# Kernel optimization log

Measured on AMD Instinct MI355X. Metric: run time of the kernel, lower is better.

The kernel has to match this reference:

```python
import jax, jax.numpy as jnp
import numpy as np

N0, N1, N2, N3 = 65536, 16384, 4096, 1024
S = 9  # 3x3 kernel -> 9 selections (self + 8 directions)


def _edges(key, n):
    # each node has S incoming edges, one per selection
    src = jax.random.randint(key, (n * S,), 0, n)
    dst = jnp.repeat(jnp.arange(n), S)
    sel = jnp.tile(jnp.arange(S), n)
    return src, dst, sel


def setup_inputs() -> dict:
    key = jax.random.key(0)
    ks = jax.random.split(key, 40)
    inp = {}
    inp["x"] = jax.random.normal(ks[0], (N0, 3), jnp.float32)
    sizes = [N0, N1, N2, N3]
    for l, n in enumerate(sizes):
        src, dst, sel = _edges(ks[1 + l], n)
        inp[f"src{l}"] = src
        inp[f"dst{l}"] = dst
        inp[f"sel{l}"] = sel
        inp[f"interp{l}"] = jax.random.uniform(ks[5 + l], (n * S,), jnp.float32)
    inp["clus0"] = jnp.arange(N0) // 4
    inp["clus1"] = jnp.arange(N1) // 4
    inp["clus2"] = jnp.arange(N2) // 4
    dims = [(3, 3), (3, 64), (64, 64), (64, 128), (128, 128), (128, 256), (256, 256), (256, 256), (256, 256), (256, 512)]
    for i, (ci, co) in enumerate(dims):
        kw = ks[10 + 2 * i]
        kb = ks[11 + 2 * i]
        if i == 0:  # conv1 is kernel_size=1 -> single weight matrix
            inp["W1"] = jax.random.normal(kw, (ci, co), jnp.float32) / np.sqrt(ci).astype(np.float32)
        else:
            inp[f"W{i + 1}"] = jax.random.normal(kw, (S, ci, co), jnp.float32) / np.sqrt(S * ci).astype(np.float32)
        inp[f"b{i + 1}"] = jax.random.normal(kb, (co,), jnp.float32) * 0.01
    return inp


def _sel_conv(x, src, dst, sel, interp, W, b):
    # message = interp * x[src]; routed to (dst, selection) bucket; per-selection weight
    n = x.shape[0]
    msg = x[src] * interp[:, None]                                  # [E, Cin]
    agg = jax.ops.segment_sum(msg, dst * S + sel, num_segments=n * S)
    agg = agg.reshape(n, S, -1)                                     # [N, S, Cin]
    return jnp.einsum('nsi,sio->no', agg, W) + b


def reference(x, src0, dst0, sel0, interp0, src1, dst1, sel1, interp1,
              src2, dst2, sel2, interp2, src3, dst3, sel3, interp3,
              clus0, clus1, clus2,
              W1, b1, W2, b2, W3, b3, W4, b4, W5, b5,
              W6, b6, W7, b7, W8, b8, W9, b9, W10, b10):
    relu = jax.nn.relu
    out = x @ W1 + b1                                              # conv1 (1x1), no relu
    r11 = relu(_sel_conv(out, src0, dst0, sel0, interp0, W2, b2))
    r12 = relu(_sel_conv(r11, src0, dst0, sel0, interp0, W3, b3))
    p1 = jax.ops.segment_max(r12, clus0, num_segments=N1)
    r21 = relu(_sel_conv(p1, src1, dst1, sel1, interp1, W4, b4))
    r22 = relu(_sel_conv(r21, src1, dst1, sel1, interp1, W5, b5))
    p2 = jax.ops.segment_max(r22, clus1, num_segments=N2)
    r31 = relu(_sel_conv(p2, src2, dst2, sel2, interp2, W6, b6))
    r32 = relu(_sel_conv(r31, src2, dst2, sel2, interp2, W7, b7))
    r33 = relu(_sel_conv(r32, src2, dst2, sel2, interp2, W8, b8))
    r34 = relu(_sel_conv(r33, src2, dst2, sel2, interp2, W9, b9))
    p3 = jax.ops.segment_max(r34, clus2, num_segments=N3)
    r41 = relu(_sel_conv(p3, src3, dst3, sel3, interp3, W10, b10))
    return (r11, r12, p1, r21, r22, p2, r31, r32, r33, r34, p3, r41)
```

## Files before the change

### kernel.cpp

```cpp
#include <hip/hip_runtime.h>
#include <hip/hip_bf16.h>
#include <cstddef>


#define S9 9

typedef __attribute__((ext_vector_type(8))) _Float16 f16x8;
typedef __attribute__((ext_vector_type(4))) float f32x4;

__device__ __forceinline__ unsigned short f2h(float f) {
    _Float16 h = (_Float16)f;
    unsigned short u;
    __builtin_memcpy(&u, &h, 2);
    return u;
}

__device__ void wt_tile(const float* __restrict__ in, unsigned short* __restrict__ out,
                        int K, int N, int t, float (*sm)[33]) {
    const int ktiles = K >> 6, ntiles = N >> 5;
    const int per = ktiles * ntiles;
    const int s = t / per;
    const int rem = t - s * per;
    const int kt = rem % ktiles, nt = rem / ktiles;
    const int k0 = kt * 64, n0 = nt * 32;
    const float* ip = in + (size_t)s * K * N;
    unsigned short* op = out + (size_t)s * N * K;
    const int tx = threadIdx.x & 31;
    const int ty = threadIdx.x >> 5;
#pragma unroll
    for (int r = ty; r < 64; r += 8)
        sm[r][tx] = ip[(size_t)(k0 + r) * N + n0 + tx];
    __syncthreads();
#pragma unroll
    for (int r = ty; r < 32; r += 8) {
        unsigned v = (unsigned)f2h(sm[2 * tx][r]) |
                     ((unsigned)f2h(sm[2 * tx + 1][r]) << 16);
        *(unsigned*)&op[(size_t)(n0 + r) * K + k0 + 2 * tx] = v;
    }
}

__global__ __launch_bounds__(256) void wt_all(
    const float* __restrict__ W2, const float* __restrict__ W3,
    const float* __restrict__ W4, const float* __restrict__ W5,
    const float* __restrict__ W6, const float* __restrict__ W7,
    const float* __restrict__ W8, const float* __restrict__ W9,
    const float* __restrict__ W10,
    unsigned short* o2, unsigned short* o3, unsigned short* o4,
    unsigned short* o5, unsigned short* o6, unsigned short* o7,
    unsigned short* o8, unsigned short* o9, unsigned short* o10) {
    __shared__ float sm[64][33];
    int b = blockIdx.x;
    if (b == 0) {
        for (int idx = threadIdx.x; idx < 64 * 32; idx += 256) {
            const int n = idx >> 5, k = idx & 31;
            o2[n * 32 + k] = (k < 27) ? f2h(W2[k * 64 + n]) : (unsigned short)0;
        }
        return;
    }
    b -= 1;
    if (b < 18)  { wt_tile(W3,  o3,  64,  64,  b, sm); return; }  b -= 18;
    if (b < 36)  { wt_tile(W4,  o4,  64,  128, b, sm); return; }  b -= 36;
    if (b < 72)  { wt_tile(W5,  o5,  128, 128, b, sm); return; }  b -= 72;
    if (b < 144) { wt_tile(W6,  o6,  128, 256, b, sm); return; }  b -= 144;
    if (b < 288) { wt_tile(W7,  o7,  256, 256, b, sm); return; }  b -= 288;
    if (b < 288) { wt_tile(W8,  o8,  256, 256, b, sm); return; }  b -= 288;
    if (b < 288) { wt_tile(W9,  o9,  256, 256, b, sm); return; }  b -= 288;
    wt_tile(W10, o10, 256, 512, b, sm);
}

__global__ void pool4_dual(const float* __restrict__ in, float* __restrict__ outf,
                           _Float16* __restrict__ outh, int total4, int C4) {
    int idx = blockIdx.x * blockDim.x + threadIdx.x;
    if (idx >= total4) return;
    int j = idx / C4;
    int c4 = idx - j * C4;
    const float4* base = (const float4*)in;
    float4 a = base[(size_t)(4 * j + 0) * C4 + c4];
    float4 b = base[(size_t)(4 * j + 1) * C4 + c4];
    float4 c = base[(size_t)(4 * j + 2) * C4 + c4];
    float4 d = base[(size_t)(4 * j + 3) * C4 + c4];
    float4 m;
    m.x = fmaxf(fmaxf(a.x, b.x), fmaxf(c.x, d.x));
    m.y = fmaxf(fmaxf(a.y, b.y), fmaxf(c.y, d.y));
    m.z = fmaxf(fmaxf(a.z, b.z), fmaxf(c.z, d.z));
    m.w = fmaxf(fmaxf(a.w, b.w), fmaxf(c.w, d.w));
    ((float4*)outf)[(size_t)j * C4 + c4] = m;
    uint2 h;
    h.x = (unsigned)f2h(m.x) | ((unsigned)f2h(m.y) << 16);
    h.y = (unsigned)f2h(m.z) | ((unsigned)f2h(m.w) << 16);
    *(uint2*)&outh[((size_t)j * C4 + c4) * 4] = h;
}

template <int BM, int WR, int WC, int MR, int NR>
__global__ __launch_bounds__(256) void selconv_k27(
    const float* __restrict__ x, const int* __restrict__ src,
    const float* __restrict__ interp, const float* __restrict__ W1,
    const float* __restrict__ b1, const _Float16* __restrict__ Wt2,
    const float* __restrict__ bias, float* __restrict__ out,
    _Float16* __restrict__ outh) {
    constexpr int COUT = 64;
    constexpr int LDA = 40;
    __shared__ _Float16 As[BM * LDA];

    const int tid = threadIdx.x;
    const int wave = tid >> 6;
    const int lane = tid & 63;
    const int wr = wave / WC;
    const int wc = wave % WC;
    const int node0 = blockIdx.x * BM;
    const int lm = lane & 15;
    const int kq = lane >> 4;

    const float w00 = W1[0], w01 = W1[1], w02 = W1[2];
    const float w10 = W1[3], w11 = W1[4], w12 = W1[5];
    const float w20 = W1[6], w21 = W1[7], w22 = W1[8];
    const float c0 = b1[0], c1 = b1[1], c2 = b1[2];

    for (int c = tid; c < BM * 5; c += 256) {
        const int ln = c / 5;
        As[ln * LDA + 27 + (c - ln * 5)] = (_Float16)0.f;
    }
    for (int c = tid; c < BM * S9; c += 256) {
        const int ln = c / S9;
        const int s = c - ln * S9;
        const int e = (node0 + ln) * S9 + s;
        const float t = interp[e];
        const float* xr = &x[(size_t)src[e] * 3];
        const float x0 = xr[0], x1 = xr[1], x2 = xr[2];
        const float y0 = fmaf(x0, w00, fmaf(x1, w10, fmaf(x2, w20, c0)));
        const float y1 = fmaf(x0, w01, fmaf(x1, w11, fmaf(x2, w21, c1)));
        const float y2 = fmaf(x0, w02, fmaf(x1, w12, fmaf(x2, w22, c2)));
        As[ln * LDA + s * 3 + 0] = (_Float16)(t * y0);
        As[ln * LDA + s * 3 + 1] = (_Float16)(t * y1);
        As[ln * LDA + s * 3 + 2] = (_Float16)(t * y2);
    }
    __syncthreads();

    f32x4 acc[MR][NR];
    f16x8 bfr[NR];
#pragma unroll
    for (int f = 0; f < NR; ++f) {
        const int col = wc * NR * 16 + f * 16 + lm;
        bfr[f] = *(const f16x8*)(Wt2 + col * 32 + kq * 8);
        const float bv = bias[col];
#pragma unroll
        for (int i = 0; i < MR; ++i) {
            acc[i][f][0] = bv; acc[i][f][1] = bv; acc[i][f][2] = bv; acc[i][f][3] = bv;
        }
    }
#pragma unroll
    for (int i = 0; i < MR; ++i) {
        const f16x8 af =
            *(const f16x8*)&As[(wr * MR * 16 + i * 16 + lm) * LDA + kq * 8];
#pragma unroll
        for (int f = 0; f < NR; ++f)
            acc[i][f] = __builtin_amdgcn_mfma_f32_16x16x32_f16(af, bfr[f],
                                                               acc[i][f], 0, 0, 0);
    }

#pragma unroll
    for (int i = 0; i < MR; ++i)
#pragma unroll
        for (int f = 0; f < NR; ++f) {
            const int col = wc * NR * 16 + f * 16 + lm;
#pragma unroll
            for (int r = 0; r < 4; ++r) {
                const int row = node0 + wr * MR * 16 + i * 16 + kq * 4 + r;
                const float v = fmaxf(acc[i][f][r], 0.f);
                out[(size_t)row * COUT + col] = v;
                outh[(size_t)row * COUT + col] = (_Float16)v;
            }
        }
}

template <int CIN, int COUT, int BM, int BNC, int WR, int WC, int MR, int NR>
__global__ __launch_bounds__(256) void selconv_f16(
    const _Float16* __restrict__ xin, const int* __restrict__ src,
    const float* __restrict__ interp, const _Float16* __restrict__ Wt,
    const float* __restrict__ bias, float* __restrict__ out,
    _Float16* __restrict__ outh) {
    static_assert(WR * WC == 4, "4 waves");
    static_assert(WR * MR * 16 == BM, "BM mismatch");
    static_assert(WC * NR * 16 == BNC, "BNC mismatch");
    constexpr int KSTEPS = CIN / 32;
    constexpr int LDA = CIN + 8;
    constexpr int C8 = CIN / 8;
    constexpr int ITER = (BM * C8) / 256;
    static_assert((BM * C8) % 256 == 0, "staging divisibility");

    __shared__ _Float16 As[BM * LDA];

    const int tid = threadIdx.x;
    const int wave = tid >> 6;
    const int lane = tid & 63;
    const int wr = wave / WC;
    const int wc = wave % WC;
    const int node0 = blockIdx.x * BM;
    const int cb = blockIdx.y * BNC;
    const int lm = lane & 15;
    const int kq = lane >> 4;

    f32x4 acc[MR][NR];
#pragma unroll
    for (int f = 0; f < NR; ++f) {
        const float bv = bias[cb + wc * NR * 16 + f * 16 + lm];
#pragma unroll
        for (int i = 0; i < MR; ++i) {
            acc[i][f][0] = bv; acc[i][f][1] = bv; acc[i][f][2] = bv; acc[i][f][3] = bv;
        }
    }

    const _Float16* __restrict__ Wb =
        Wt + ((size_t)cb + wc * NR * 16 + lm) * CIN + kq * 8;

#pragma unroll 1
    for (int s = 0; s < S9; ++s) {
        int sidx[ITER];
        float ta[ITER];
#pragma unroll
        for (int i = 0; i < ITER; ++i) {
            const int c = tid + i * 256;
            const int ln = c / C8;
            const int e = (node0 + ln) * S9 + s;
            sidx[i] = src[e];
            ta[i] = interp[e];
        }
        f16x8 va[ITER];
#pragma unroll
        for (int i = 0; i < ITER; ++i) {
            const int c = tid + i * 256;
            const int c8 = c - (c / C8) * C8;
            va[i] = *(const f16x8*)&xin[(size_t)sidx[i] * CIN + c8 * 8];
        }
        f16x8 bfr[KSTEPS][NR];
        {
            const _Float16* __restrict__ Wbs = Wb + (size_t)s * COUT * CIN;
#pragma unroll
            for (int kk = 0; kk < KSTEPS; ++kk)
#pragma unroll
                for (int f = 0; f < NR; ++f)
                    bfr[kk][f] = *(const f16x8*)(Wbs + (size_t)f * 16 * CIN + kk * 32);
        }
        __syncthreads();
#pragma unroll
        for (int i = 0; i < ITER; ++i) {
            const int c = tid + i * 256;
            const int ln = c / C8;
            const int c8 = c - ln * C8;
            const _Float16 ht = (_Float16)ta[i];
            f16x8 r;
#pragma unroll
            for (int j = 0; j < 8; ++j) r[j] = va[i][j] * ht;
            *(f16x8*)&As[ln * LDA + c8 * 8] = r;
        }
        __syncthreads();
#pragma unroll
        for (int kk = 0; kk < KSTEPS; ++kk) {
            f16x8 af[MR];
#pragma unroll
            for (int i = 0; i < MR; ++i)
                af[i] = *(const f16x8*)&As[(wr * MR * 16 + i * 16 + lm) * LDA +
                                           kk * 32 + kq * 8];
#pragma unroll
            for (int i = 0; i < MR; ++i)
#pragma unroll
                for (int f = 0; f < NR; ++f)
                    acc[i][f] = __builtin_amdgcn_mfma_f32_16x16x32_f16(
                        af[i], bfr[kk][f], acc[i][f], 0, 0, 0);
        }
    }

#pragma unroll
    for (int i = 0; i < MR; ++i)
#pragma unroll
        for (int f = 0; f < NR; ++f) {
            const int col = cb + wc * NR * 16 + f * 16 + lm;
#pragma unroll
            for (int r = 0; r < 4; ++r) {
                const int row = node0 + wr * MR * 16 + i * 16 + kq * 4 + r;
                const float v = fmaxf(acc[i][f][r], 0.f);
                out[(size_t)row * COUT + col] = v;
                if (outh) outh[(size_t)row * COUT + col] = (_Float16)v;
            }
        }
}

extern "C" void kernel_launch(void* const* d_in, const int* in_sizes, int n_in,
                              void* d_out, int out_size, void* d_ws, size_t ws_size,
                              hipStream_t stream) {
    const float* x = (const float*)d_in[0];
    const int* src0 = (const int*)d_in[1];
    const float* interp0 = (const float*)d_in[4];
    const int* src1 = (const int*)d_in[5];
    const float* interp1 = (const float*)d_in[8];
    const int* src2 = (const int*)d_in[9];
    const float* interp2 = (const float*)d_in[12];
    const int* src3 = (const int*)d_in[13];
    const float* interp3 = (const float*)d_in[16];
    const float* W1 = (const float*)d_in[20];
    const float* b1 = (const float*)d_in[21];
    const float* W2 = (const float*)d_in[22];
    const float* b2 = (const float*)d_in[23];
    const float* W3 = (const float*)d_in[24];
    const float* b3 = (const float*)d_in[25];
    const float* W4 = (const float*)d_in[26];
    const float* b4 = (const float*)d_in[27];
    const float* W5 = (const float*)d_in[28];
    const float* b5 = (const float*)d_in[29];
    const float* W6 = (const float*)d_in[30];
    const float* b6 = (const float*)d_in[31];
    const float* W7 = (const float*)d_in[32];
    const float* b7 = (const float*)d_in[33];
    const float* W8 = (const float*)d_in[34];
    const float* b8 = (const float*)d_in[35];
    const float* W9 = (const float*)d_in[36];
    const float* b9 = (const float*)d_in[37];
    const float* W10 = (const float*)d_in[38];
    const float* b10 = (const float*)d_in[39];

    float* out = (float*)d_out;
    float* r11 = out;
    float* r12 = r11 + (size_t)65536 * 64;
    float* p1 = r12 + (size_t)65536 * 64;
    float* r21 = p1 + (size_t)16384 * 64;
    float* r22 = r21 + (size_t)16384 * 128;
    float* p2 = r22 + (size_t)16384 * 128;
    float* r31 = p2 + (size_t)4096 * 128;
    float* r32 = r31 + (size_t)4096 * 256;
    float* r33 = r32 + (size_t)4096 * 256;
    float* r34 = r33 + (size_t)4096 * 256;
    float* p3 = r34 + (size_t)4096 * 256;
    float* r41 = p3 + (size_t)1024 * 256;

    unsigned short* w16 = (unsigned short*)d_ws;
    unsigned short* Wt2 = w16;
    unsigned short* Wt3 = Wt2 + (size_t)64 * 32;
    unsigned short* Wt4 = Wt3 + (size_t)9 * 64 * 64;
    unsigned short* Wt5 = Wt4 + (size_t)9 * 128 * 64;
    unsigned short* Wt6 = Wt5 + (size_t)9 * 128 * 128;
    unsigned short* Wt7 = Wt6 + (size_t)9 * 256 * 128;
    unsigned short* Wt8 = Wt7 + (size_t)9 * 256 * 256;
    unsigned short* Wt9 = Wt8 + (size_t)9 * 256 * 256;
    unsigned short* Wt10 = Wt9 + (size_t)9 * 256 * 256;
    unsigned short* endw = Wt10 + (size_t)9 * 512 * 256;
    _Float16* a11 = (_Float16*)endw;
    _Float16* ap1 = a11 + (size_t)65536 * 64;
    _Float16* a21 = ap1 + (size_t)16384 * 64;
    _Float16* ap2 = a21 + (size_t)16384 * 128;
    _Float16* a31 = ap2 + (size_t)4096 * 128;
    _Float16* a32 = a31 + (size_t)4096 * 256;
    _Float16* a33 = a32 + (size_t)4096 * 256;
    _Float16* ap3 = a33 + (size_t)4096 * 256;

    wt_all<<<1711, 256, 0, stream>>>(W2, W3, W4, W5, W6, W7, W8, W9, W10,
                                     Wt2, Wt3, Wt4, Wt5, Wt6, Wt7, Wt8, Wt9, Wt10);

    selconv_k27<64, 2, 2, 2, 2><<<dim3(65536 / 64), 256, 0, stream>>>(
        x, src0, interp0, W1, b1, (const _Float16*)Wt2, b2, r11, a11);

    selconv_f16<64, 64, 64, 64, 2, 2, 2, 2><<<dim3(65536 / 64, 1), 256, 0, stream>>>(
        a11, src0, interp0, (const _Float16*)Wt3, b3, r12, nullptr);
    pool4_dual<<<(16384 * 16 + 255) / 256, 256, 0, stream>>>(r12, p1, ap1,
                                                             16384 * 16, 16);

    selconv_f16<64, 128, 32, 64, 2, 2, 1, 2><<<dim3(16384 / 32, 2), 256, 0, stream>>>(
        ap1, src1, interp1, (const _Float16*)Wt4, b4, r21, a21);
    selconv_f16<128, 128, 32, 64, 2, 2, 1, 2><<<dim3(16384 / 32, 2), 256, 0, stream>>>(
        a21, src1, interp1, (const _Float16*)Wt5, b5, r22, nullptr);
    pool4_dual<<<(4096 * 32 + 255) / 256, 256, 0, stream>>>(r22, p2, ap2,
                                                            4096 * 32, 32);

    selconv_f16<128, 256, 32, 64, 2, 2, 1, 2><<<dim3(4096 / 32, 4), 256, 0, stream>>>(
        ap2, src2, interp2, (const _Float16*)Wt6, b6, r31, a31);
    selconv_f16<256, 256, 32, 64, 2, 2, 1, 2><<<dim3(4096 / 32, 4), 256, 0, stream>>>(
        a31, src2, interp2, (const _Float16*)Wt7, b7, r32, a32);
    selconv_f16<256, 256, 32, 64, 2, 2, 1, 2><<<dim3(4096 / 32, 4), 256, 0, stream>>>(
        a32, src2, interp2, (const _Float16*)Wt8, b8, r33, a33);
    selconv_f16<256, 256, 32, 64, 2, 2, 1, 2><<<dim3(4096 / 32, 4), 256, 0, stream>>>(
        a33, src2, interp2, (const _Float16*)Wt9, b9, r34, nullptr);
    pool4_dual<<<(1024 * 64 + 255) / 256, 256, 0, stream>>>(r34, p3, ap3,
                                                            1024 * 64, 64);

    selconv_f16<256, 512, 16, 64, 1, 4, 1, 1><<<dim3(1024 / 16, 8), 256, 0, stream>>>(
        ap3, src3, interp3, (const _Float16*)Wt10, b10, r41, nullptr);
}
```

Before: 430.5 us.

## Gather MFMA operands directly into registers and fuse max-pool into conv epilogue

Removes the shared-memory staging and both barriers in the selection conv kernel. Each lane now gathers its A-fragment rows straight from global memory, scales them by interp in registers, and prefetches the next selection's src and interp values. The separate pool4 kernels are dropped: the 4 accumulator rows a lane holds (kq*4..+3) are max-reduced in the epilogue to write the pooled fp32 and fp16 outputs. Tile sizes are also unified to BM=64, which cuts grid sizes on the small layers (16 or 64 row blocks) and may reduce occupancy. The uncoalesced per-lane gathers (16-byte chunks per lane) could cost memory efficiency.

Result: no change. 433.0 us (+0.6%).

```diff
diff --git a/kernel.cpp b/kernel.cpp
--- a/kernel.cpp
+++ b/kernel.cpp
@@ -68,29 +68,6 @@
     wt_tile(W10, o10, 256, 512, b, sm);
 }
 
-__global__ void pool4_dual(const float* __restrict__ in, float* __restrict__ outf,
-                           _Float16* __restrict__ outh, int total4, int C4) {
-    int idx = blockIdx.x * blockDim.x + threadIdx.x;
-    if (idx >= total4) return;
-    int j = idx / C4;
-    int c4 = idx - j * C4;
-    const float4* base = (const float4*)in;
-    float4 a = base[(size_t)(4 * j + 0) * C4 + c4];
-    float4 b = base[(size_t)(4 * j + 1) * C4 + c4];
-    float4 c = base[(size_t)(4 * j + 2) * C4 + c4];
-    float4 d = base[(size_t)(4 * j + 3) * C4 + c4];
-    float4 m;
-    m.x = fmaxf(fmaxf(a.x, b.x), fmaxf(c.x, d.x));
-    m.y = fmaxf(fmaxf(a.y, b.y), fmaxf(c.y, d.y));
-    m.z = fmaxf(fmaxf(a.z, b.z), fmaxf(c.z, d.z));
-    m.w = fmaxf(fmaxf(a.w, b.w), fmaxf(c.w, d.w));
-    ((float4*)outf)[(size_t)j * C4 + c4] = m;
-    uint2 h;
-    h.x = (unsigned)f2h(m.x) | ((unsigned)f2h(m.y) << 16);
-    h.y = (unsigned)f2h(m.z) | ((unsigned)f2h(m.w) << 16);
-    *(uint2*)&outh[((size_t)j * C4 + c4) * 4] = h;
-}
-
 template <int BM, int WR, int WC, int MR, int NR>
 __global__ __launch_bounds__(256) void selconv_k27(
     const float* __restrict__ x, const int* __restrict__ src,
@@ -173,22 +150,19 @@
         }
 }
 
-template <int CIN, int COUT, int BM, int BNC, int WR, int WC, int MR, int NR>
-__global__ __launch_bounds__(256) void selconv_f16(
+template <int CIN, int COUT, int BM, int BNC, int WR, int WC, int MR, int NR,
+          bool POOL>
+__global__ __launch_bounds__(256) void selconv_dir(
     const _Float16* __restrict__ xin, const int* __restrict__ src,
     const float* __restrict__ interp, const _Float16* __restrict__ Wt,
     const float* __restrict__ bias, float* __restrict__ out,
-    _Float16* __restrict__ outh) {
+    _Float16* __restrict__ outh, float* __restrict__ pout,
+    _Float16* __restrict__ ph) {
     static_assert(WR * WC == 4, "4 waves");
     static_assert(WR * MR * 16 == BM, "BM mismatch");
     static_assert(WC * NR * 16 == BNC, "BNC mismatch");
     constexpr int KSTEPS = CIN / 32;
-    constexpr int LDA = CIN + 8;
-    constexpr int C8 = CIN / 8;
-    constexpr int ITER = (BM * C8) / 256;
-    static_assert((BM * C8) % 256 == 0, "staging divisibility");
-
-    __shared__ _Float16 As[BM * LDA];
+    static_assert(CIN % 32 == 0, "CIN multiple of 32");
 
     const int tid = threadIdx.x;
     const int wave = tid >> 6;
@@ -206,67 +180,75 @@
         const float bv = bias[cb + wc * NR * 16 + f * 16 + lm];
 #pragma unroll
         for (int i = 0; i < MR; ++i) {
-            acc[i][f][0] = bv; acc[i][f][1] = bv; acc[i][f][2] = bv; acc[i][f][3] = bv;
+            acc[i][f][0] = bv; acc[i][f][1] = bv;
+            acc[i][f][2] = bv; acc[i][f][3] = bv;
         }
     }
 
     const _Float16* __restrict__ Wb =
         Wt + ((size_t)cb + wc * NR * 16 + lm) * CIN + kq * 8;
 
+    int ebase[MR];
+#pragma unroll
+    for (int i = 0; i < MR; ++i)
+        ebase[i] = (node0 + (wr * MR + i) * 16 + lm) * S9;
+
+    int se_c[MR];
+    float ti_c[MR];
+#pragma unroll
+    for (int i = 0; i < MR; ++i) {
+        se_c[i] = src[ebase[i]];
+        ti_c[i] = interp[ebase[i]];
+    }
+
 #pragma unroll 1
     for (int s = 0; s < S9; ++s) {
-        int sidx[ITER];
-        float ta[ITER];
-#pragma unroll
-        for (int i = 0; i < ITER; ++i) {
-            const int c = tid + i * 256;
-            const int ln = c / C8;
-            const int e = (node0 + ln) * S9 + s;
-            sidx[i] = src[e];
-            ta[i] = interp[e];
-        }
-        f16x8 va[ITER];
-#pragma unroll
-        for (int i = 0; i < ITER; ++i) {
-            const int c = tid + i * 256;
-            const int c8 = c - (c / C8) * C8;
-            va[i] = *(const f16x8*)&xin[(size_t)sidx[i] * CIN + c8 * 8];
-        }
+        const int sn = (s + 1 < S9) ? s + 1 : s;
+        int se_n[MR];
+        float ti_n[MR];
+#pragma unroll
+        for (int i = 0; i < MR; ++i) {
+            se_n[i] = src[ebase[i] + sn];
+            ti_n[i] = interp[ebase[i] + sn];
+        }
+
+        const _Float16* __restrict__ Ws = Wb + (size_t)s * COUT * CIN;
         f16x8 bfr[KSTEPS][NR];
-        {
-            const _Float16* __restrict__ Wbs = Wb + (size_t)s * COUT * CIN;
+#pragma unroll
+        for (int kk = 0; kk < KSTEPS; ++kk)
+#pragma unroll
+            for (int f = 0; f < NR; ++f)
+                bfr[kk][f] = *(const f16x8*)(Ws + (size_t)f * 16 * CIN + kk * 32);
+
+        f16x8 av[MR][KSTEPS];
+#pragma unroll
+        for (int i = 0; i < MR; ++i) {
+            const _Float16* __restrict__ xr =
+                xin + (size_t)se_c[i] * CIN + kq * 8;
 #pragma unroll
             for (int kk = 0; kk < KSTEPS; ++kk)
-#pragma unroll
-                for (int f = 0; f < NR; ++f)
-                    bfr[kk][f] = *(const f16x8*)(Wbs + (size_t)f * 16 * CIN + kk * 32);
-        }
-        __syncthreads();
-#pragma unroll
-        for (int i = 0; i < ITER; ++i) {
-            const int c = tid + i * 256;
-            const int ln = c / C8;
-            const int c8 = c - ln * C8;
-            const _Float16 ht = (_Float16)ta[i];
-            f16x8 r;
-#pragma unroll
-            for (int j = 0; j < 8; ++j) r[j] = va[i][j] * ht;
-            *(f16x8*)&As[ln * LDA + c8 * 8] = r;
-        }
-        __syncthreads();
-#pragma unroll
-        for (int kk = 0; kk < KSTEPS; ++kk) {
-            f16x8 af[MR];
-#pragma unroll
-            for (int i = 0; i < MR; ++i)
-                af[i] = *(const f16x8*)&As[(wr * MR * 16 + i * 16 + lm) * LDA +
-                                           kk * 32 + kq * 8];
-#pragma unroll
-            for (int i = 0; i < MR; ++i)
+                av[i][kk] = *(const f16x8*)(xr + kk * 32);
+        }
+
+#pragma unroll
+        for (int i = 0; i < MR; ++i) {
+            const _Float16 t = (_Float16)ti_c[i];
+#pragma unroll
+            for (int kk = 0; kk < KSTEPS; ++kk) {
+                f16x8 a = av[i][kk];
+#pragma unroll
+                for (int j = 0; j < 8; ++j) a[j] *= t;
 #pragma unroll
                 for (int f = 0; f < NR; ++f)
                     acc[i][f] = __builtin_amdgcn_mfma_f32_16x16x32_f16(
-                        af[i], bfr[kk][f], acc[i][f], 0, 0, 0);
+                        a, bfr[kk][f], acc[i][f], 0, 0, 0);
+            }
+        }
+
+#pragma unroll
+        for (int i = 0; i < MR; ++i) {
+            se_c[i] = se_n[i];
+            ti_c[i] = ti_n[i];
         }
     }
 
@@ -275,12 +257,26 @@
 #pragma unroll
         for (int f = 0; f < NR; ++f) {
             const int col = cb + wc * NR * 16 + f * 16 + lm;
-#pragma unroll
-            for (int r = 0; r < 4; ++r) {
-                const int row = node0 + wr * MR * 16 + i * 16 + kq * 4 + r;
-                const float v = fmaxf(acc[i][f][r], 0.f);
-                out[(size_t)row * COUT + col] = v;
-                if (outh) outh[(size_t)row * COUT + col] = (_Float16)v;
+            const int rb = node0 + (wr * MR + i) * 16 + kq * 4;
+            float v0 = fmaxf(acc[i][f][0], 0.f);
+            float v1 = fmaxf(acc[i][f][1], 0.f);
+            float v2 = fmaxf(acc[i][f][2], 0.f);
+            float v3 = fmaxf(acc[i][f][3], 0.f);
+            out[(size_t)(rb + 0) * COUT + col] = v0;
+            out[(size_t)(rb + 1) * COUT + col] = v1;
+            out[(size_t)(rb + 2) * COUT + col] = v2;
+            out[(size_t)(rb + 3) * COUT + col] = v3;
+            if (outh) {
+                outh[(size_t)(rb + 0) * COUT + col] = (_Float16)v0;
+                outh[(size_t)(rb + 1) * COUT + col] = (_Float16)v1;
+                outh[(size_t)(rb + 2) * COUT + col] = (_Float16)v2;
+                outh[(size_t)(rb + 3) * COUT + col] = (_Float16)v3;
+            }
+            if constexpr (POOL) {
+                const float m = fmaxf(fmaxf(v0, v1), fmaxf(v2, v3));
+                const int prow = rb >> 2;
+                pout[(size_t)prow * COUT + col] = m;
+                ph[(size_t)prow * COUT + col] = (_Float16)m;
             }
         }
 }
@@ -358,29 +354,32 @@
     selconv_k27<64, 2, 2, 2, 2><<<dim3(65536 / 64), 256, 0, stream>>>(
         x, src0, interp0, W1, b1, (const _Float16*)Wt2, b2, r11, a11);
 
-    selconv_f16<64, 64, 64, 64, 2, 2, 2, 2><<<dim3(65536 / 64, 1), 256, 0, stream>>>(
-        a11, src0, interp0, (const _Float16*)Wt3, b3, r12, nullptr);
-    pool4_dual<<<(16384 * 16 + 255) / 256, 256, 0, stream>>>(r12, p1, ap1,
-                                                             16384 * 16, 16);
-
-    selconv_f16<64, 128, 32, 64, 2, 2, 1, 2><<<dim3(16384 / 32, 2), 256, 0, stream>>>(
-        ap1, src1, interp1, (const _Float16*)Wt4, b4, r21, a21);
-    selconv_f16<128, 128, 32, 64, 2, 2, 1, 2><<<dim3(16384 / 32, 2), 256, 0, stream>>>(
-        a21, src1, interp1, (const _Float16*)Wt5, b5, r22, nullptr);
-    pool4_dual<<<(4096 * 32 + 255) / 256, 256, 0, stream>>>(r22, p2, ap2,
-                                                            4096 * 32, 32);
-
-    selconv_f16<128, 256, 32, 64, 2, 2, 1, 2><<<dim3(4096 / 32, 4), 256, 0, stream>>>(
-        ap2, src2, interp2, (const _Float16*)Wt6, b6, r31, a31);
-    selconv_f16<256, 256, 32, 64, 2, 2, 1, 2><<<dim3(4096 / 32, 4), 256, 0, stream>>>(
-        a31, src2, interp2, (const _Float16*)Wt7, b7, r32, a32);
-    selconv_f16<256, 256, 32, 64, 2, 2, 1, 2><<<dim3(4096 / 32, 4), 256, 0, stream>>>(
-        a32, src2, interp2, (const _Float16*)Wt8, b8, r33, a33);
-    selconv_f16<256, 256, 32, 64, 2, 2, 1, 2><<<dim3(4096 / 32, 4), 256, 0, stream>>>(
-        a33, src2, interp2, (const _Float16*)Wt9, b9, r34, nullptr);
-    pool4_dual<<<(1024 * 64 + 255) / 256, 256, 0, stream>>>(r34, p3, ap3,
-                                                            1024 * 64, 64);
-
-    selconv_f16<256, 512, 16, 64, 1, 4, 1, 1><<<dim3(1024 / 16, 8), 256, 0, stream>>>(
-        ap3, src3, interp3, (const _Float16*)Wt10, b10, r41, nullptr);
-}
+    selconv_dir<64, 64, 64, 64, 2, 2, 2, 2, true>
+        <<<dim3(1024, 1), 256, 0, stream>>>(
+            a11, src0, interp0, (const _Float16*)Wt3, b3, r12, nullptr, p1, ap1);
+
+    selconv_dir<64, 128, 64, 64, 2, 2, 2, 2, false>
+        <<<dim3(256, 2), 256, 0, stream>>>(
+            ap1, src1, interp1, (const _Float16*)Wt4, b4, r21, a21, nullptr, nullptr);
+
+    selconv_dir<128, 128, 64, 64, 2, 2, 2, 2, true>
+        <<<dim3(256, 2), 256, 0, stream>>>(
+            a21, src1, interp1, (const _Float16*)Wt5, b5, r22, nullptr, p2, ap2);
+
+    selconv_dir<128, 256, 64, 64, 2, 2, 2, 2, false>
+        <<<dim3(64, 4), 256, 0, stream>>>(
+            ap2, src2, interp2, (const _Float16*)Wt6, b6, r31, a31, nullptr, nullptr);
+    selconv_dir<256, 256, 64, 64, 2, 2, 2, 2, false>
+        <<<dim3(64, 4), 256, 0, stream>>>(
+            a31, src2, interp2, (const _Float16*)Wt7, b7, r32, a32, nullptr, nullptr);
+    selconv_dir<256, 256, 64, 64, 2, 2, 2, 2, false>
+        <<<dim3(64, 4), 256, 0, stream>>>(
+            a32, src2, interp2, (const _Float16*)Wt8, b8, r33, a33, nullptr, nullptr);
+    selconv_dir<256, 256, 64, 64, 2, 2, 2, 2, true>
+        <<<dim3(64, 4), 256, 0, stream>>>(
+            a33, src2, interp2, (const _Float16*)Wt9, b9, r34, nullptr, p3, ap3);
+
+    selconv_dir<256, 512, 64, 64, 2, 2, 2, 2, false>
+        <<<dim3(16, 8), 256, 0, stream>>>(
+            ap3, src3, interp3, (const _Float16*)Wt10, b10, r41, nullptr, nullptr, nullptr);
+}
```
